# Kernel optimization log

Hardware: AMD Instinct MI355X
Metric: run time of the kernel (lower is better)

The kernel has to match this reference:

```python
import jax, jax.numpy as jnp
import numpy as np

N_NODES = 100000
N_EDGES = 1600000
N_GRAPHS = 64
D_IN = 3
HIDDEN = 256
N_CLASSES = 10
NEG_SLOPE = 0.01  # torch F.leaky_relu default


def gcn_conv(x, W, b, src, dst, n_nodes):
    """GCNConv: D^{-1/2}(A+I)D^{-1/2} X W + b with self-loops."""
    h = x @ W  # [N, H]
    ones = jnp.ones(src.shape[0], h.dtype)
    deg = jax.ops.segment_sum(ones, dst, num_segments=n_nodes) + 1.0  # +1 self-loop
    dinv = jax.lax.rsqrt(deg)
    coef = dinv[src] * dinv[dst]  # [E]
    agg = jax.ops.segment_sum(h[src] * coef[:, None], dst, num_segments=n_nodes)
    agg = agg + h * (1.0 / deg)[:, None]  # self-loop contribution (norm = 1/deg)
    return agg + b


def leaky_relu(v):
    return jnp.where(v >= 0, v, NEG_SLOPE * v)


def setup_inputs() -> dict:
    key = jax.random.key(0)
    ks = jax.random.split(key, 12)
    x = jax.random.normal(ks[0], (N_NODES, D_IN), dtype=jnp.float32)
    edge_index = jax.random.randint(ks[1], (2, N_EDGES), 0, N_NODES, dtype=jnp.int32)
    batch = jnp.sort(jax.random.randint(ks[2], (N_NODES,), 0, N_GRAPHS, dtype=jnp.int32))
    s1 = 1.0 / np.sqrt(D_IN)
    s2 = 1.0 / np.sqrt(HIDDEN)
    W1 = jax.random.uniform(ks[3], (D_IN, HIDDEN), jnp.float32, -s1, s1)
    b1 = jnp.zeros((HIDDEN,), jnp.float32)
    W2 = jax.random.uniform(ks[4], (HIDDEN, HIDDEN), jnp.float32, -s2, s2)
    b2 = jnp.zeros((HIDDEN,), jnp.float32)
    W3 = jax.random.uniform(ks[5], (HIDDEN, HIDDEN), jnp.float32, -s2, s2)
    b3 = jnp.zeros((HIDDEN,), jnp.float32)
    Wc = jax.random.uniform(ks[6], (HIDDEN, N_CLASSES), jnp.float32, -s2, s2)
    bc = jax.random.uniform(ks[7], (N_CLASSES,), jnp.float32, -s2, s2)
    return {"x": x, "edge_index": edge_index, "batch": batch,
            "W1": W1, "b1": b1, "W2": W2, "b2": b2, "W3": W3, "b3": b3,
            "Wc": Wc, "bc": bc}


def reference(x, edge_index, batch, W1, b1, W2, b2, W3, b3, Wc, bc):
    src, dst = edge_index[0], edge_index[1]
    h = leaky_relu(gcn_conv(x, W1, b1, src, dst, N_NODES))
    h = leaky_relu(gcn_conv(h, W2, b2, src, dst, N_NODES))
    h = leaky_relu(gcn_conv(h, W3, b3, src, dst, N_NODES))
    # global mean pool over graphs
    sums = jax.ops.segment_sum(h, batch, num_segments=N_GRAPHS)
    cnt = jax.ops.segment_sum(jnp.ones((N_NODES,), h.dtype), batch, num_segments=N_GRAPHS)
    pooled = sums / jnp.maximum(cnt, 1.0)[:, None]  # [G, H]
    logits = pooled @ Wc + bc
    return jax.nn.softmax(logits, axis=1)
```

## Files before the change

### kernel.cpp

```cpp
#include <hip/hip_runtime.h>
#include <hip/hip_bf16.h>
#include <hip/hip_fp16.h>
#include <cstdint>
#include <cstddef>

#define N_NODES   100000
#define N_EDGES   1600000
#define N_GRAPHS  64
#define HIDDEN    256
#define N_CLASSES 10
#define NEG_SLOPE 0.01f

#define E_PAD    (N_EDGES + 8 * N_NODES)
#define GEMM_BLOCKS 391

#define PART_EDGES  8192
#define PART_BLOCKS ((N_EDGES + PART_EDGES - 1) / PART_EDGES)
#define SUB_BITS 10
#define SUB_SIZE 1024
#define N_SUB    ((N_NODES + SUB_SIZE - 1) / SUB_SIZE)
#define CAP_SUB  17408

typedef __attribute__((ext_vector_type(4))) float f32x4;
typedef __attribute__((ext_vector_type(2))) float f32x2;

__device__ __forceinline__ float bf2f(unsigned short u) {
    return __uint_as_float(((unsigned int)u) << 16);
}

__device__ __forceinline__ unsigned char f2fp8(float v) {
    return (unsigned char)(__builtin_amdgcn_cvt_pk_fp8_f32(v, v, 0, false) & 0xff);
}

__device__ __forceinline__ unsigned int rec_pack(int s, float c) {
    __half h = __float2half(c);
    unsigned short hb = reinterpret_cast<const __half_raw*>(&h)->x;
    return ((unsigned int)hb << 17) | (unsigned int)s;
}
__device__ __forceinline__ float rec_coef(unsigned int u) {
    __half_raw hr; hr.x = (unsigned short)(u >> 17);
    return __half2float(*reinterpret_cast<const __half*>(&hr));
}

__global__ __launch_bounds__(256) void k_partition(const int* __restrict__ src, const int* __restrict__ dst,
                                                   int* __restrict__ gcur, unsigned int* __restrict__ bucket) {
    __shared__ int lcnt[N_SUB];
    __shared__ int lbase[N_SUB];
    __shared__ int gbase[N_SUB];
    __shared__ unsigned int stage[PART_EDGES];
    int tid = threadIdx.x;
    for (int i = tid; i < N_SUB; i += 256) lcnt[i] = 0;
    __syncthreads();
    int e0 = blockIdx.x * PART_EDGES + tid * 8;
    for (int g = 0; g < 4; ++g) {
        int e = e0 + g * 2048;
        if (e < N_EDGES) {
            int4 da = *(const int4*)(dst + e);
            int4 db = *(const int4*)(dst + e + 4);
            int d[8] = {da.x, da.y, da.z, da.w, db.x, db.y, db.z, db.w};
#pragma unroll
            for (int j = 0; j < 8; ++j) atomicAdd(&lcnt[d[j] >> SUB_BITS], 1);
        }
    }
    __syncthreads();
    if (tid == 0) {
        int s = 0;
        for (int r = 0; r < N_SUB; ++r) { lbase[r] = s; s += lcnt[r]; }
    }
    __syncthreads();
    for (int i = tid; i < N_SUB; i += 256) {
        gbase[i] = atomicAdd(&gcur[i * 16], lcnt[i]);
        lcnt[i] = lbase[i];
    }
    __syncthreads();
    for (int g = 0; g < 4; ++g) {
        int e = e0 + g * 2048;
        if (e < N_EDGES) {
            int4 da = *(const int4*)(dst + e);
            int4 db = *(const int4*)(dst + e + 4);
            int4 sa = *(const int4*)(src + e);
            int4 sb = *(const int4*)(src + e + 4);
            int d[8] = {da.x, da.y, da.z, da.w, db.x, db.y, db.z, db.w};
            int s[8] = {sa.x, sa.y, sa.z, sa.w, sb.x, sb.y, sb.z, sb.w};
#pragma unroll
            for (int j = 0; j < 8; ++j) {
                int r = d[j] >> SUB_BITS;
                int p = atomicAdd(&lcnt[r], 1);
                stage[p] = ((unsigned int)(d[j] & (SUB_SIZE - 1)) << 17) | (unsigned int)s[j];
            }
        }
    }
    __syncthreads();
    int wv = tid >> 6, ln = tid & 63;
    for (int r = wv; r < N_SUB; r += 4) {
        int base = lbase[r], n = lcnt[r] - base, gb = gbase[r];
        unsigned int* dp = bucket + (size_t)r * CAP_SUB + gb;
        for (int k = ln; k < n; k += 64) dp[k] = stage[base + k];
    }
}

__global__ __launch_bounds__(512) void k_hist3(const unsigned int* __restrict__ bucket,
                                               const int* __restrict__ gcur, int* __restrict__ cnt) {
    int sub = blockIdx.x;
    __shared__ int hist[SUB_SIZE];
    for (int i = threadIdx.x; i < SUB_SIZE; i += 512) hist[i] = 0;
    __syncthreads();
    int n = gcur[sub * 16];
    const unsigned int* bp = bucket + (size_t)sub * CAP_SUB;
    for (int i0 = threadIdx.x * 8; i0 < n; i0 += 512 * 8) {
        uint4 ua = *(const uint4*)(bp + i0);
        uint4 ub = *(const uint4*)(bp + i0 + 4);
        unsigned int u[8] = {ua.x, ua.y, ua.z, ua.w, ub.x, ub.y, ub.z, ub.w};
        int m = n - i0; if (m > 8) m = 8;
#pragma unroll
        for (int j = 0; j < 8; ++j) if (j < m) atomicAdd(&hist[u[j] >> 17], 1);
    }
    __syncthreads();
    int base = sub * SUB_SIZE;
    for (int i = threadIdx.x; i < SUB_SIZE; i += 512)
        if (base + i < N_NODES) cnt[base + i] = hist[i];
}

__global__ __launch_bounds__(512) void k_fill3(const unsigned int* __restrict__ bucket,
                                               const int* __restrict__ gcur,
                                               const float* __restrict__ dinv,
                                               const int* __restrict__ off,
                                               unsigned int* __restrict__ rec) {
    int sub = blockIdx.x;
    __shared__ int lcur[SUB_SIZE];
    __shared__ float ldv[SUB_SIZE];
    int nb0 = sub * SUB_SIZE;
    for (int i = threadIdx.x; i < SUB_SIZE; i += 512) {
        int node = nb0 + i;
        lcur[i] = (node < N_NODES) ? off[node] : 0;
        ldv[i]  = (node < N_NODES) ? dinv[node] : 0.f;
    }
    __syncthreads();
    int n = gcur[sub * 16];
    const unsigned int* bp = bucket + (size_t)sub * CAP_SUB;
    for (int i0 = threadIdx.x * 8; i0 < n; i0 += 512 * 8) {
        uint4 ua = *(const uint4*)(bp + i0);
        uint4 ub = *(const uint4*)(bp + i0 + 4);
        unsigned int u[8] = {ua.x, ua.y, ua.z, ua.w, ub.x, ub.y, ub.z, ub.w};
        int m = n - i0; if (m > 8) m = 8;
        float ds[8];
#pragma unroll
        for (int j = 0; j < 8; ++j) {
            int s = (j < m) ? (int)(u[j] & 0x1ffff) : 0;
            ds[j] = dinv[s];
        }
#pragma unroll
        for (int j = 0; j < 8; ++j) {
            if (j < m) {
                int dr = (int)(u[j] >> 17);
                float c = ds[j] * ldv[dr];
                int p = atomicAdd(&lcur[dr], 1);
                rec[p] = rec_pack((int)(u[j] & 0x1ffff), c);
            }
        }
    }
}

__global__ void k_graph_bounds(const int* __restrict__ batch,
                               int* __restrict__ gstart, int* __restrict__ gcnt) {
    int g = threadIdx.x;
    int lo = 0, hi = N_NODES;
    while (lo < hi) { int mid = (lo + hi) >> 1; if (batch[mid] < g) lo = mid + 1; else hi = mid; }
    __shared__ int sh[N_GRAPHS + 1];
    sh[g] = lo;
    if (g == 0) sh[N_GRAPHS] = N_NODES;
    __syncthreads();
    gstart[g] = sh[g];
    gcnt[g]   = sh[g + 1] - sh[g];
}

__global__ void k_dinv_xpad(const int* __restrict__ cnt, const float* __restrict__ x,
                            float* __restrict__ dinv, float4* __restrict__ xp) {
    int i = blockIdx.x * 256 + threadIdx.x;
    if (i < N_NODES) {
        dinv[i] = rsqrtf((float)cnt[i] + 1.0f);
        xp[i] = make_float4(x[i * 3 + 0], x[i * 3 + 1], x[i * 3 + 2], 0.f);
    }
}

__global__ void k_scanA(const int* __restrict__ cnt, int* __restrict__ out, int* __restrict__ bsum) {
    __shared__ int sh[256];
    int tid = threadIdx.x;
    int base = blockIdx.x * 1024 + tid * 4;
    int v[4]; int s = 0;
#pragma unroll
    for (int i = 0; i < 4; i++) {
        int idx = base + i;
        v[i] = (idx < N_NODES) ? ((cnt[idx] + 7) & ~7) : 0;
        s += v[i];
    }
    sh[tid] = s; __syncthreads();
    for (int off = 1; off < 256; off <<= 1) {
        int t = (tid >= off) ? sh[tid - off] : 0;
        __syncthreads();
        sh[tid] += t;
        __syncthreads();
    }
    int excl = sh[tid] - s;
    if (tid == 255) bsum[blockIdx.x] = sh[255];
#pragma unroll
    for (int i = 0; i < 4; i++) { int idx = base + i; if (idx < N_NODES) out[idx] = excl; excl += v[i]; }
}

__global__ void k_scanB(int* __restrict__ bsum, int nb) {
    __shared__ int sh[128];
    int tid = threadIdx.x;
    int v = (tid < nb) ? bsum[tid] : 0;
    sh[tid] = v; __syncthreads();
    for (int off = 1; off < 128; off <<= 1) {
        int t = (tid >= off) ? sh[tid - off] : 0;
        __syncthreads();
        sh[tid] += t;
        __syncthreads();
    }
    if (tid < nb) bsum[tid] = sh[tid] - v;
}

__global__ void k_scanC(int* __restrict__ off_arr, const int* __restrict__ bsum,
                        const int* __restrict__ cnt, unsigned int* __restrict__ rec) {
    int i = blockIdx.x * 256 + threadIdx.x;
    if (i < N_NODES) {
        int v = off_arr[i] + bsum[i >> 10];
        off_arr[i] = v;
        int c  = cnt[i];
        int cp = (c + 7) & ~7;
        for (int p = v + c; p < v + cp; ++p) rec[p] = 0u;
        if (i == N_NODES - 1) off_arr[N_NODES] = v + cp;
    }
}

__global__ void k_wprep(const float* __restrict__ W, unsigned char* __restrict__ Wswz) {
    int n = blockIdx.x; int k = threadIdx.x;
    unsigned char v = f2fp8(W[k * HIDDEN + n]);
    int k0 = k >> 5, nt = n >> 4;
    int lane = (((k >> 3) & 3) << 4) | (n & 15);
    int j = k & 7;
    Wswz[(size_t)(((k0 * 16) + nt) * 64 + lane) * 8 + j] = v;
}

__global__ void k_agg3(const float4* __restrict__ xp, const int* __restrict__ off,
                       const unsigned int* __restrict__ rec, const float* __restrict__ dinv,
                       float4* __restrict__ ax) {
    int i = blockIdx.x * 256 + threadIdx.x;
    if (i >= N_NODES) return;
    float di = dinv[i];
    float selfc = di * di;
    float4 xi = xp[i];
    float a0 = xi.x * selfc, a1 = xi.y * selfc, a2 = xi.z * selfc;
    int e = off[i], e1 = off[i + 1];
    for (; e < e1; e += 4) {
        uint4 rr = *(const uint4*)(rec + e);
        int s0 = rr.x & 0x1ffff, s1 = rr.y & 0x1ffff, s2 = rr.z & 0x1ffff, s3 = rr.w & 0x1ffff;
        float c0 = rec_coef(rr.x), c1 = rec_coef(rr.y), c2 = rec_coef(rr.z), c3 = rec_coef(rr.w);
        float4 x0 = xp[s0], x1 = xp[s1], x2 = xp[s2], x3 = xp[s3];
        a0 += c0 * x0.x + c1 * x1.x + c2 * x2.x + c3 * x3.x;
        a1 += c0 * x0.y + c1 * x1.y + c2 * x2.y + c3 * x3.y;
        a2 += c0 * x0.z + c1 * x1.z + c2 * x2.z + c3 * x3.z;
    }
    ax[i] = make_float4(a0, a1, a2, 0.f);
}

__global__ void k_l1(const float4* __restrict__ ax, const float* __restrict__ W1,
                     const float* __restrict__ b1, unsigned char* __restrict__ out) {
    int node = blockIdx.x; int c = threadIdx.x;
    float4 a = ax[node];
    float v = a.x * W1[c] + a.y * W1[HIDDEN + c] + a.z * W1[2 * HIDDEN + c] + b1[c];
    v = v >= 0.f ? v : NEG_SLOPE * v;
    out[(size_t)node * HIDDEN + c] = f2fp8(v);
}

__global__ __launch_bounds__(512, 2) void k_gemm_mfma(const unsigned char* __restrict__ A,
                                                      const unsigned char* __restrict__ Wswz,
                                                      unsigned char* __restrict__ C, int M) {
    __shared__ long Bs[8192];
    int tid = threadIdx.x;
    {
        const float4* gsrc = (const float4*)Wswz;
        float4* ldst = (float4*)Bs;
#pragma unroll
        for (int i = 0; i < 8; ++i) ldst[tid + 512 * i] = gsrc[tid + 512 * i];
    }
    __syncthreads();
    int lane = tid & 63, wv = tid >> 6;
    int quad = lane >> 4, r = lane & 15;
    int nstrips = M >> 4;
    for (int s = blockIdx.x * 8 + wv; s < nstrips; s += gridDim.x * 8) {
        int m0 = s * 16;
        const long* Ab = (const long*)(A + (size_t)(m0 + r) * HIDDEN) + quad;
        long af[8];
#pragma unroll
        for (int k0 = 0; k0 < 8; ++k0) af[k0] = Ab[k0 * 4];
        f32x4 acc[16];
#pragma unroll
        for (int i = 0; i < 16; i++) acc[i] = (f32x4){0.f, 0.f, 0.f, 0.f};
#pragma unroll
        for (int k0 = 0; k0 < 8; ++k0) {
#pragma unroll
            for (int nt = 0; nt < 16; ++nt) {
                long w = Bs[(k0 * 16 + nt) * 64 + lane];
                acc[nt] = __builtin_amdgcn_mfma_f32_16x16x32_fp8_fp8(w, af[k0], acc[nt], 0, 0, 0);
            }
        }
        unsigned int* crow = (unsigned int*)(C + (size_t)(m0 + r) * HIDDEN + quad * 4);
#pragma unroll
        for (int nt = 0; nt < 16; ++nt) {
            unsigned int pk = __builtin_amdgcn_cvt_pk_fp8_f32(acc[nt][0], acc[nt][1], 0, false);
            pk = __builtin_amdgcn_cvt_pk_fp8_f32(acc[nt][2], acc[nt][3], pk, true);
            crow[nt * 4] = pk;
        }
    }
}

__global__ __launch_bounds__(256) void k_agg(const unsigned char* __restrict__ h,
                                             const float* __restrict__ bias,
                                             const int* __restrict__ off, const unsigned int* __restrict__ rec,
                                             const float* __restrict__ dinv,
                                             unsigned char* __restrict__ out) {
    int node = (blockIdx.x * 256 + threadIdx.x) >> 6;
    int lane = threadIdx.x & 63;
    if (node >= N_NODES) return;
    float di = dinv[node];
    float selfc = di * di;
    unsigned int hv = *(const unsigned int*)(h + (size_t)node * HIDDEN + lane * 4);
    f32x2 hlo = __builtin_amdgcn_cvt_pk_f32_fp8(hv, false);
    f32x2 hhi = __builtin_amdgcn_cvt_pk_f32_fp8(hv, true);
    float4 bv = ((const float4*)bias)[lane];
    float4 acc = make_float4(bv.x + hlo.x * selfc, bv.y + hlo.y * selfc,
                             bv.z + hhi.x * selfc, bv.w + hhi.y * selfc);
    int e = off[node], e1 = off[node + 1];
    for (; e < e1; e += 8) {
        uint4 ra = *(const uint4*)(rec + e);
        uint4 rb = *(const uint4*)(rec + e + 4);
        unsigned int w0 = *(const unsigned int*)(h + (size_t)(ra.x & 0x1ffff) * HIDDEN + lane * 4);
        unsigned int w1 = *(const unsigned int*)(h + (size_t)(ra.y & 0x1ffff) * HIDDEN + lane * 4);
        unsigned int w2 = *(const unsigned int*)(h + (size_t)(ra.z & 0x1ffff) * HIDDEN + lane * 4);
        unsigned int w3 = *(const unsigned int*)(h + (size_t)(ra.w & 0x1ffff) * HIDDEN + lane * 4);
        unsigned int w4 = *(const unsigned int*)(h + (size_t)(rb.x & 0x1ffff) * HIDDEN + lane * 4);
        unsigned int w5 = *(const unsigned int*)(h + (size_t)(rb.y & 0x1ffff) * HIDDEN + lane * 4);
        unsigned int w6 = *(const unsigned int*)(h + (size_t)(rb.z & 0x1ffff) * HIDDEN + lane * 4);
        unsigned int w7 = *(const unsigned int*)(h + (size_t)(rb.w & 0x1ffff) * HIDDEN + lane * 4);
        float c0 = rec_coef(ra.x), c1 = rec_coef(ra.y), c2 = rec_coef(ra.z), c3 = rec_coef(ra.w);
        float c4 = rec_coef(rb.x), c5 = rec_coef(rb.y), c6 = rec_coef(rb.z), c7 = rec_coef(rb.w);
        f32x2 l0 = __builtin_amdgcn_cvt_pk_f32_fp8(w0, false), g0 = __builtin_amdgcn_cvt_pk_f32_fp8(w0, true);
        f32x2 l1 = __builtin_amdgcn_cvt_pk_f32_fp8(w1, false), g1 = __builtin_amdgcn_cvt_pk_f32_fp8(w1, true);
        f32x2 l2 = __builtin_amdgcn_cvt_pk_f32_fp8(w2, false), g2 = __builtin_amdgcn_cvt_pk_f32_fp8(w2, true);
        f32x2 l3 = __builtin_amdgcn_cvt_pk_f32_fp8(w3, false), g3 = __builtin_amdgcn_cvt_pk_f32_fp8(w3, true);
        f32x2 l4 = __builtin_amdgcn_cvt_pk_f32_fp8(w4, false), g4 = __builtin_amdgcn_cvt_pk_f32_fp8(w4, true);
        f32x2 l5 = __builtin_amdgcn_cvt_pk_f32_fp8(w5, false), g5 = __builtin_amdgcn_cvt_pk_f32_fp8(w5, true);
        f32x2 l6 = __builtin_amdgcn_cvt_pk_f32_fp8(w6, false), g6 = __builtin_amdgcn_cvt_pk_f32_fp8(w6, true);
        f32x2 l7 = __builtin_amdgcn_cvt_pk_f32_fp8(w7, false), g7 = __builtin_amdgcn_cvt_pk_f32_fp8(w7, true);
        acc.x += c0 * l0.x + c1 * l1.x + c2 * l2.x + c3 * l3.x
               + c4 * l4.x + c5 * l5.x + c6 * l6.x + c7 * l7.x;
        acc.y += c0 * l0.y + c1 * l1.y + c2 * l2.y + c3 * l3.y
               + c4 * l4.y + c5 * l5.y + c6 * l6.y + c7 * l7.y;
        acc.z += c0 * g0.x + c1 * g1.x + c2 * g2.x + c3 * g3.x
               + c4 * g4.x + c5 * g5.x + c6 * g6.x + c7 * g7.x;
        acc.w += c0 * g0.y + c1 * g1.y + c2 * g2.y + c3 * g3.y
               + c4 * g4.y + c5 * g5.y + c6 * g6.y + c7 * g7.y;
    }
    acc.x = acc.x >= 0.f ? acc.x : NEG_SLOPE * acc.x;
    acc.y = acc.y >= 0.f ? acc.y : NEG_SLOPE * acc.y;
    acc.z = acc.z >= 0.f ? acc.z : NEG_SLOPE * acc.z;
    acc.w = acc.w >= 0.f ? acc.w : NEG_SLOPE * acc.w;
    unsigned int pk = __builtin_amdgcn_cvt_pk_fp8_f32(acc.x, acc.y, 0, false);
    pk = __builtin_amdgcn_cvt_pk_fp8_f32(acc.z, acc.w, pk, true);
    *(unsigned int*)(out + (size_t)node * HIDDEN + lane * 4) = pk;
}

__global__ void k_pool(const unsigned char* __restrict__ h, const int* __restrict__ gstart,
                       const int* __restrict__ gcnt, float* __restrict__ pooled) {
    int g = blockIdx.x, chunk = blockIdx.y, t = threadIdx.x;
    int s = gstart[g], c = gcnt[g];
    int i0 = s + (int)(((long long)c * chunk) / 16);
    int i1 = s + (int)(((long long)c * (chunk + 1)) / 16);
    float acc = 0.f;
    for (int i = i0; i < i1; ++i) {
        f32x2 v = __builtin_amdgcn_cvt_pk_f32_fp8((unsigned int)h[(size_t)i * HIDDEN + t], false);
        acc += v.x;
    }
    atomicAdd(&pooled[g * HIDDEN + t], acc);
}

__global__ void k_head(const float* __restrict__ pooled, const int* __restrict__ gcnt,
                       const float* __restrict__ Wc, const float* __restrict__ bc,
                       float* __restrict__ out) {
    int g = blockIdx.x; int l = threadIdx.x;
    float inv = 1.0f / fmaxf((float)gcnt[g], 1.0f);
    float p[4];
#pragma unroll
    for (int i = 0; i < 4; i++) p[i] = pooled[g * HIDDEN + l + i * 64] * inv;
    __shared__ float logits[N_CLASSES];
#pragma unroll
    for (int j = 0; j < N_CLASSES; j++) {
        float s = 0.f;
#pragma unroll
        for (int i = 0; i < 4; i++) s += p[i] * Wc[(l + i * 64) * N_CLASSES + j];
        for (int o = 32; o > 0; o >>= 1) s += __shfl_down(s, o, 64);
        if (l == 0) logits[j] = s + bc[j];
    }
    __syncthreads();
    if (l == 0) {
        float m = logits[0];
        for (int j = 1; j < N_CLASSES; j++) m = fmaxf(m, logits[j]);
        float e[N_CLASSES]; float sum = 0.f;
        for (int j = 0; j < N_CLASSES; j++) { e[j] = expf(logits[j] - m); sum += e[j]; }
        for (int j = 0; j < N_CLASSES; j++) out[g * N_CLASSES + j] = e[j] / sum;
    }
}

extern "C" void kernel_launch(void* const* d_in, const int* in_sizes, int n_in,
                              void* d_out, int out_size, void* d_ws, size_t ws_size,
                              hipStream_t stream) {
    const float* x     = (const float*)d_in[0];
    const int*   edge  = (const int*)d_in[1];
    const int*   batch = (const int*)d_in[2];
    const float* W1 = (const float*)d_in[3];
    const float* b1 = (const float*)d_in[4];
    const float* W2 = (const float*)d_in[5];
    const float* b2 = (const float*)d_in[6];
    const float* W3 = (const float*)d_in[7];
    const float* b3 = (const float*)d_in[8];
    const float* Wc = (const float*)d_in[9];
    const float* bc = (const float*)d_in[10];
    float* out = (float*)d_out;
    const int* srcp = edge;
    const int* dstp = edge + N_EDGES;

    char* ws = (char*)d_ws;
    size_t off = 0;
    auto alloc = [&](size_t bytes) -> char* {
        char* p = ws + off;
        off += (bytes + 255) & ~(size_t)255;
        return p;
    };
    unsigned char* hA   = (unsigned char*)alloc((size_t)N_NODES * HIDDEN);
    unsigned char* hB   = (unsigned char*)alloc((size_t)N_NODES * HIDDEN);
    unsigned char* Wz2  = (unsigned char*)alloc((size_t)HIDDEN * HIDDEN);
    unsigned char* Wz3  = (unsigned char*)alloc((size_t)HIDDEN * HIDDEN);
    int*   deg_cnt  = (int*)alloc((size_t)N_NODES * 4);
    float* dinv     = (float*)alloc((size_t)N_NODES * 4);
    int*   csr_off  = (int*)alloc((size_t)(N_NODES + 1) * 4);
    unsigned int* csr_rec = (unsigned int*)alloc((size_t)E_PAD * 4);
    float4* ax      = (float4*)alloc((size_t)N_NODES * 16);
    float4* xp      = (float4*)alloc((size_t)N_NODES * 16);
    int*   gcnt     = (int*)alloc((size_t)N_GRAPHS * 4);
    int*   gstart   = (int*)alloc((size_t)N_GRAPHS * 4);
    float* pooled   = (float*)alloc((size_t)N_GRAPHS * HIDDEN * 4);
    int*   bsum     = (int*)alloc(128 * 4);
    int*   gcur     = (int*)alloc((size_t)N_SUB * 16 * 4);

    unsigned int* bucket = (unsigned int*)hB;

    hipMemsetAsync(gcur, 0, (size_t)N_SUB * 16 * 4, stream);
    hipMemsetAsync(pooled, 0, (size_t)N_GRAPHS * HIDDEN * 4, stream);

    int nb  = (N_NODES + 255) / 256;
    int sblocks = (N_NODES + 1023) / 1024;

    k_partition<<<PART_BLOCKS, 256, 0, stream>>>(srcp, dstp, gcur, bucket);
    k_graph_bounds<<<1, 64, 0, stream>>>(batch, gstart, gcnt);
    k_hist3<<<N_SUB, 512, 0, stream>>>(bucket, gcur, deg_cnt);
    k_dinv_xpad<<<nb, 256, 0, stream>>>(deg_cnt, x, dinv, xp);
    k_scanA<<<sblocks, 256, 0, stream>>>(deg_cnt, csr_off, bsum);
    k_scanB<<<1, 128, 0, stream>>>(bsum, sblocks);
    k_scanC<<<nb, 256, 0, stream>>>(csr_off, bsum, deg_cnt, csr_rec);
    k_fill3<<<N_SUB, 512, 0, stream>>>(bucket, gcur, dinv, csr_off, csr_rec);
    k_wprep<<<HIDDEN, HIDDEN, 0, stream>>>(W2, Wz2);
    k_wprep<<<HIDDEN, HIDDEN, 0, stream>>>(W3, Wz3);

    k_agg3<<<nb, 256, 0, stream>>>(xp, csr_off, csr_rec, dinv, ax);
    k_l1<<<N_NODES, 256, 0, stream>>>(ax, W1, b1, hA);

    int aggb = (N_NODES + 3) / 4;
    k_gemm_mfma<<<GEMM_BLOCKS, 512, 0, stream>>>(hA, Wz2, hB, N_NODES);
    k_agg<<<aggb, 256, 0, stream>>>(hB, b2, csr_off, csr_rec, dinv, hA);
    k_gemm_mfma<<<GEMM_BLOCKS, 512, 0, stream>>>(hA, Wz3, hB, N_NODES);
    k_agg<<<aggb, 256, 0, stream>>>(hB, b3, csr_off, csr_rec, dinv, hA);
    dim3 pg(N_GRAPHS, 16);
    k_pool<<<pg, 256, 0, stream>>>(hA, gstart, gcnt, pooled);
    k_head<<<N_GRAPHS, 64, 0, stream>>>(pooled, gcnt, Wc, bc, out);
}
```

Before: 478.5 us.

## Use atomic work-stealing and LDS-staged coalesced stores in FP8 MFMA GEMM

Replaces the static strided strip assignment in the FP8 MFMA GEMM with a per-wave atomic counter that hands out 16-row strips dynamically, and raises the grid to 512 blocks. Output is now staged through a per-wave LDS tile so each lane writes 16 contiguous bytes instead of scattered 4-byte stores. The aim is better load balance across CUs and more coalesced global writes. It adds one global atomic per strip, extra LDS traffic, and two counters that must be zeroed by a memset before the launches.

```diff
diff --git a/kernel.cpp b/kernel.cpp
--- a/kernel.cpp
+++ b/kernel.cpp
@@ -12,7 +12,7 @@
 #define NEG_SLOPE 0.01f
 
 #define E_PAD    (N_EDGES + 8 * N_NODES)
-#define GEMM_BLOCKS 391
+#define GEMM_BLOCKS 512
 
 #define PART_EDGES  8192
 #define PART_BLOCKS ((N_EDGES + PART_EDGES - 1) / PART_EDGES)
@@ -276,8 +276,10 @@
 
 __global__ __launch_bounds__(512, 2) void k_gemm_mfma(const unsigned char* __restrict__ A,
                                                       const unsigned char* __restrict__ Wswz,
-                                                      unsigned char* __restrict__ C, int M) {
+                                                      unsigned char* __restrict__ C, int M,
+                                                      int* __restrict__ ctr) {
     __shared__ long Bs[8192];
+    __shared__ unsigned int St[8][320];
     int tid = threadIdx.x;
     {
         const float4* gsrc = (const float4*)Wswz;
@@ -289,7 +291,13 @@
     int lane = tid & 63, wv = tid >> 6;
     int quad = lane >> 4, r = lane & 15;
     int nstrips = M >> 4;
-    for (int s = blockIdx.x * 8 + wv; s < nstrips; s += gridDim.x * 8) {
+    unsigned int* stw = &St[wv][0];
+    int rrow = lane >> 2, rseg = lane & 3;
+    for (;;) {
+        int s = 0;
+        if (lane == 0) s = atomicAdd(ctr, 1);
+        s = __shfl(s, 0, 64);
+        if (s >= nstrips) break;
         int m0 = s * 16;
         const long* Ab = (const long*)(A + (size_t)(m0 + r) * HIDDEN) + quad;
         long af[8];
@@ -306,12 +314,17 @@
                 acc[nt] = __builtin_amdgcn_mfma_f32_16x16x32_fp8_fp8(w, af[k0], acc[nt], 0, 0, 0);
             }
         }
-        unsigned int* crow = (unsigned int*)(C + (size_t)(m0 + r) * HIDDEN + quad * 4);
-#pragma unroll
-        for (int nt = 0; nt < 16; ++nt) {
-            unsigned int pk = __builtin_amdgcn_cvt_pk_fp8_f32(acc[nt][0], acc[nt][1], 0, false);
-            pk = __builtin_amdgcn_cvt_pk_fp8_f32(acc[nt][2], acc[nt][3], pk, true);
-            crow[nt * 4] = pk;
+#pragma unroll
+        for (int q4 = 0; q4 < 4; ++q4) {
+#pragma unroll
+            for (int t = 0; t < 4; ++t) {
+                f32x4 a = acc[q4 * 4 + t];
+                unsigned int pk = __builtin_amdgcn_cvt_pk_fp8_f32(a[0], a[1], 0, false);
+                pk = __builtin_amdgcn_cvt_pk_fp8_f32(a[2], a[3], pk, true);
+                stw[r * 20 + t * 4 + quad] = pk;
+            }
+            uint4 v = *(const uint4*)&stw[rrow * 20 + rseg * 4];
+            *(uint4*)(C + (size_t)(m0 + rrow) * HIDDEN + q4 * 64 + rseg * 16) = v;
         }
     }
 }
@@ -453,10 +466,12 @@
     float* pooled   = (float*)alloc((size_t)N_GRAPHS * HIDDEN * 4);
     int*   bsum     = (int*)alloc(128 * 4);
     int*   gcur     = (int*)alloc((size_t)N_SUB * 16 * 4);
+    int*   gemmctr  = (int*)alloc(512);
 
     unsigned int* bucket = (unsigned int*)hB;
 
     hipMemsetAsync(gcur, 0, (size_t)N_SUB * 16 * 4, stream);
+    hipMemsetAsync(gemmctr, 0, 512, stream);
     hipMemsetAsync(pooled, 0, (size_t)N_GRAPHS * HIDDEN * 4, stream);
 
     int nb  = (N_NODES + 255) / 256;
@@ -477,9 +492,9 @@
     k_l1<<<N_NODES, 256, 0, stream>>>(ax, W1, b1, hA);
 
     int aggb = (N_NODES + 3) / 4;
-    k_gemm_mfma<<<GEMM_BLOCKS, 512, 0, stream>>>(hA, Wz2, hB, N_NODES);
+    k_gemm_mfma<<<GEMM_BLOCKS, 512, 0, stream>>>(hA, Wz2, hB, N_NODES, gemmctr);
     k_agg<<<aggb, 256, 0, stream>>>(hB, b2, csr_off, csr_rec, dinv, hA);
-    k_gemm_mfma<<<GEMM_BLOCKS, 512, 0, stream>>>(hA, Wz3, hB, N_NODES);
+    k_gemm_mfma<<<GEMM_BLOCKS, 512, 0, stream>>>(hA, Wz3, hB, N_NODES, gemmctr + 64);
     k_agg<<<aggb, 256, 0, stream>>>(hB, b3, csr_off, csr_rec, dinv, hA);
     dim3 pg(N_GRAPHS, 16);
     k_pool<<<pg, 256, 0, stream>>>(hA, gstart, gcnt, pooled);
```

Result: slower. 593.2 us (+24.0%).
